# Kernel tuning notes

Measured on AMD Instinct MI355X. Metric: run time of the kernel, lower is better.

The kernel has to match this reference:

```python
import jax, jax.numpy as jnp
import numpy as np

B, L, D, NHEAD, NLAYERS = 2, 2048, 256, 8, 8
NAMES = ['self', 'cross'] * 4


def setup_inputs() -> dict:
    key = jax.random.key(0)
    ks = jax.random.split(key, 6)
    w_scale = D ** -0.5  # keep activations well-scaled
    return {
        'f0': jax.random.normal(ks[0], (B, L, D), dtype=jnp.float32),
        'f1': jax.random.normal(ks[1], (B, L, D), dtype=jnp.float32),
        'Wq': jax.random.normal(ks[2], (NLAYERS, D, D), dtype=jnp.float32) * w_scale,
        'Wk': jax.random.normal(ks[3], (NLAYERS, D, D), dtype=jnp.float32) * w_scale,
        'Wv': jax.random.normal(ks[4], (NLAYERS, D, D), dtype=jnp.float32) * w_scale,
        'Wo': jax.random.normal(ks[5], (NLAYERS, D, D), dtype=jnp.float32) * w_scale,
    }


def _rope(x, inv_freq):
    # x: (B, L, D); RoPE over the FULL model dim (matches original, mixes heads)
    L_, D_ = x.shape[1], x.shape[2]
    t = jnp.arange(L_, dtype=jnp.float32)
    freqs = t[:, None] * inv_freq[None, :]          # (L, D/2)
    emb = jnp.concatenate([freqs, freqs], axis=-1)  # (L, D)
    x1, x2 = x[..., : D_ // 2], x[..., D_ // 2:]
    rot = jnp.concatenate([-x2, x1], axis=-1)
    return x * jnp.cos(emb) + rot * jnp.sin(emb)


def _attn(x, src, wq, wk, wv, wo, use_rope, inv_freq):
    b, l1, d = x.shape
    l2 = src.shape[1]
    dh = d // NHEAD
    q = x @ wq.T    # torch Linear: x @ W^T
    k = src @ wk.T
    v = src @ wv.T
    if use_rope:
        q = _rope(q, inv_freq)
        k = _rope(k, inv_freq)
    q = q.reshape(b, l1, NHEAD, dh)
    k = k.reshape(b, l2, NHEAD, dh)
    v = v.reshape(b, l2, NHEAD, dh)
    scores = jnp.einsum('bqhd,bkhd->bhqk', q, k) * (dh ** -0.5)
    out = jnp.einsum('bhqk,bkhd->bqhd', jax.nn.softmax(scores, axis=-1), v)
    return out.reshape(b, l1, d) @ wo.T


def reference(f0, f1, Wq, Wk, Wv, Wo):
    d = f0.shape[-1]
    inv_freq = 1.0 / (10000.0 ** (jnp.arange(0, d, 2, dtype=jnp.float32) / d))
    for i, name in enumerate(NAMES):
        if name == 'self':
            f0 = f0 + _attn(f0, f0, Wq[i], Wk[i], Wv[i], Wo[i], True, inv_freq)
            f1 = f1 + _attn(f1, f1, Wq[i], Wk[i], Wv[i], Wo[i], True, inv_freq)
        else:
            # sequential updates: second cross uses the UPDATED f0 (matches torch)
            f0 = f0 + _attn(f0, f1, Wq[i], Wk[i], Wv[i], Wo[i], False, inv_freq)
            f1 = f1 + _attn(f1, f0, Wq[i], Wk[i], Wv[i], Wo[i], False, inv_freq)
    return (f0, f1)
```

## Files before the change

kernel.cpp:

```cpp
#include <hip/hip_runtime.h>

#define BB   2
#define LL   2048
#define DD   256
#define NH   8
#define MM   (BB*LL)
#define NLAYERS 8
#define MMDD ((size_t)MM*DD)

typedef unsigned short ushort_t;
typedef __attribute__((ext_vector_type(8))) short  short8;
typedef __attribute__((ext_vector_type(4))) float  f32x4;
typedef __attribute__((ext_vector_type(4))) unsigned int u32x4;
typedef __attribute__((ext_vector_type(2))) unsigned int u32x2;

#define CSC 0.2550500394f

#define WAITV0 asm volatile("s_waitcnt vmcnt(0)" ::: "memory")
#define WAITV2 asm volatile("s_waitcnt vmcnt(2)" ::: "memory")
#define WAITV4 asm volatile("s_waitcnt vmcnt(4)" ::: "memory")
#define WAITV6 asm volatile("s_waitcnt vmcnt(6)" ::: "memory")
#define WAITLG asm volatile("s_waitcnt lgkmcnt(0)" ::: "memory")
#define BAR()  __builtin_amdgcn_s_barrier()
#define SCHED0 __builtin_amdgcn_sched_barrier(0)

__device__ __forceinline__ f32x4 mfma16(short8 a, short8 b, f32x4 c) {
    return __builtin_amdgcn_mfma_f32_16x16x32_bf16(a, b, c, 0, 0, 0);
}
__device__ __forceinline__ unsigned cvtpk(float lo, float hi) {
    unsigned r;
    asm volatile("v_cvt_pk_bf16_f32 %0, %1, %2" : "=v"(r) : "v"(lo), "v"(hi));
    return r;
}
__device__ __forceinline__ void pl32(unsigned &a, unsigned &b) {
    asm volatile("v_permlane32_swap_b32 %0, %1" : "+v"(a), "+v"(b));
}
__device__ __forceinline__ float bf2f(unsigned short h) {
    return __builtin_bit_cast(float, ((unsigned)h) << 16);
}
__device__ __forceinline__ void gll16(const void* gsrc, void* ldst) {
    __builtin_amdgcn_global_load_lds(
        (const __attribute__((address_space(1))) unsigned int*)gsrc,
        (__attribute__((address_space(3))) unsigned int*)ldst, 16, 0, 0);
}


__global__ __launch_bounds__(256) void setup(const float* __restrict__ f0,
                                             const float* __restrict__ f1,
                                             const float* __restrict__ Wq,
                                             const float* __restrict__ Wk,
                                             const float* __restrict__ Wv,
                                             const float* __restrict__ Wo,
                                             float* __restrict__ F,
                                             ushort_t* __restrict__ Fb,
                                             ushort_t* __restrict__ Wb,
                                             float* __restrict__ tab) {
    int b = blockIdx.x, t = threadIdx.x;
    if (b < 1024) {
        int i = b * 256 + t;
        const float* src = (i < 131072) ? f0 : f1;
        int loc = i & 131071;
        const f32x4* p = (const f32x4*)(src + (size_t)loc * 8);
        f32x4 a = p[0], bb = p[1];
        *(f32x4*)&F[(size_t)i * 8]     = a;
        *(f32x4*)&F[(size_t)i * 8 + 4] = bb;
        u32x4 o = {cvtpk(a.x, a.y), cvtpk(a.z, a.w), cvtpk(bb.x, bb.y), cvtpk(bb.z, bb.w)};
        *(u32x4*)&Fb[(size_t)i * 8] = o;
    } else if (b < 2048) {
        int i = (b - 1024) * 256 + t;
        int reg = i >> 16, loc = i & 65535;
        const float* src = reg == 0 ? Wq : reg == 1 ? Wk : reg == 2 ? Wv : Wo;
        const f32x4* p = (const f32x4*)(src + (size_t)loc * 8);
        f32x4 x = p[0], y = p[1];
        u32x4 o = {cvtpk(x.x, x.y), cvtpk(x.z, x.w), cvtpk(y.x, y.y), cvtpk(y.z, y.w)};
        *(u32x4*)&Wb[(size_t)reg * 524288 + (size_t)loc * 8] = o;
    } else {
        int idx = (b - 2048) * 256 + t;
        int p = idx >> 7, j = idx & 127;
        float inv = __expf(-((float)j / 128.f) * 9.210340371976184f);
        float s, c;
        sincosf((float)p * inv, &s, &c);
        tab[(size_t)p * 256 + j]       = c;
        tab[(size_t)p * 256 + 128 + j] = s;
    }
}

__global__ __launch_bounds__(256) void gemmQK(const ushort_t* __restrict__ X,
                                              const ushort_t* __restrict__ WQ,
                                              const ushort_t* __restrict__ WK,
                                              ushort_t* __restrict__ DQ,
                                              ushort_t* __restrict__ KT,
                                              const float* __restrict__ tab) {
    __shared__ ushort_t Xb[2][4096];
    __shared__ ushort_t WbL[2][4096];
    __shared__ ushort_t WbH[2][4096];
    const int tid = threadIdx.x, ln = tid & 63, w = tid >> 6;
    const int f = blockIdx.x;
    const int xcd = f & 7, u = f >> 3;
    const int bx = u & 3, byg = u >> 2;
    const int mat = bx >> 1, cg = bx & 1;
    const int by = xcd * 16 + byg;
    const int m0 = by * 64, n0 = cg * 64;
    const ushort_t* W = mat ? WK : WQ;

    auto stage = [&](int c, int buf) {
#pragma unroll
        for (int i = 0; i < 2; i++) {
            int sl = (w * 2 + i) * 64 + ln;
            int r = sl >> 3, x = sl & 7;
            int col = c * 64 + ((x ^ (r & 7)) << 3);
            gll16(X + (size_t)(m0 + r) * 256 + col,       &Xb[buf][(w * 2 + i) * 512]);
            gll16(W + (size_t)(n0 + r) * 256 + col,       &WbL[buf][(w * 2 + i) * 512]);
            gll16(W + (size_t)(n0 + 128 + r) * 256 + col, &WbH[buf][(w * 2 + i) * 512]);
        }
    };

    const int ql = ln & 15, gq = ln >> 4;
    const int wm = w >> 1, wn = w & 1;
    f32x4 z4 = {0.f, 0.f, 0.f, 0.f};
    f32x4 accL[2][2] = {{z4, z4}, {z4, z4}};
    f32x4 accH[2][2] = {{z4, z4}, {z4, z4}};

    stage(0, 0);
    stage(1, 1);
#pragma unroll
    for (int c = 0; c < 4; c++) {
        if (c < 3) { WAITV6; } else { WAITV0; }
        BAR(); SCHED0;
        const ushort_t* XL = Xb[c & 1];
        const ushort_t* WL = WbL[c & 1];
        const ushort_t* WH = WbH[c & 1];
        __builtin_amdgcn_s_setprio(1);
#pragma unroll
        for (int ks = 0; ks < 2; ks++) {
            int cc = ks * 4 + gq;
            int r0 = 32 * wm + ql, r1 = r0 + 16;
            int nr0 = 32 * wn + ql, nr1 = nr0 + 16;
            short8 a0 = *(const short8*)&XL[(r0 * 8 + (cc ^ (r0 & 7))) * 8];
            short8 a1 = *(const short8*)&XL[(r1 * 8 + (cc ^ (r1 & 7))) * 8];
            short8 l0 = *(const short8*)&WL[(nr0 * 8 + (cc ^ (nr0 & 7))) * 8];
            short8 l1 = *(const short8*)&WL[(nr1 * 8 + (cc ^ (nr1 & 7))) * 8];
            short8 h0 = *(const short8*)&WH[(nr0 * 8 + (cc ^ (nr0 & 7))) * 8];
            short8 h1 = *(const short8*)&WH[(nr1 * 8 + (cc ^ (nr1 & 7))) * 8];
            accL[0][0] = mfma16(a0, l0, accL[0][0]);
            accL[0][1] = mfma16(a0, l1, accL[0][1]);
            accL[1][0] = mfma16(a1, l0, accL[1][0]);
            accL[1][1] = mfma16(a1, l1, accL[1][1]);
            accH[0][0] = mfma16(a0, h0, accH[0][0]);
            accH[0][1] = mfma16(a0, h1, accH[0][1]);
            accH[1][0] = mfma16(a1, h0, accH[1][0]);
            accH[1][1] = mfma16(a1, h1, accH[1][1]);
        }
        __builtin_amdgcn_s_setprio(0);
        BAR();
        if (c + 2 < 4) stage(c + 2, c & 1);
    }

#pragma unroll
    for (int mf = 0; mf < 2; mf++)
#pragma unroll
        for (int nf = 0; nf < 2; nf++)
#pragma unroll
            for (int r = 0; r < 4; r++) {
                int mg = m0 + 32 * wm + 16 * mf + gq * 4 + r;
                int jl = n0 + 32 * wn + 16 * nf + ql;
                int pos = mg & (LL - 1);
                float a = accL[mf][nf][r], b = accH[mf][nf][r];
                float c = tab[(size_t)pos * 256 + jl];
                float s = tab[(size_t)pos * 256 + 128 + jl];
                float o1 = a * c - b * s;
                float o2 = b * c + a * s;
                if (mat == 0) {
                    o1 *= CSC; o2 *= CSC;
                    DQ[(size_t)mg * 256 + jl]       = (ushort_t)cvtpk(o1, o1);
                    DQ[(size_t)mg * 256 + jl + 128] = (ushort_t)cvtpk(o2, o2);
                } else {
                    int z = mg >> 11, key = mg & 2047;
                    int tt = key >> 6, kk = key & 63;
                    int dh = jl & 31, hA = jl >> 5;
                    size_t base = (size_t)tt * 2048 + (size_t)(dh >> 3) * 512
                                + (size_t)kk * 8 + (dh & 7);
                    KT[(size_t)(z * 8 + hA) * 65536 + base]     = (ushort_t)cvtpk(o1, o1);
                    KT[(size_t)(z * 8 + hA + 4) * 65536 + base] = (ushort_t)cvtpk(o2, o2);
                }
            }
}

template<int NQ, int NK, int NV, int QMODE, int KMODE, int NTY>
__global__ __launch_bounds__(256) void gemm5(const ushort_t* __restrict__ X,
                                             const ushort_t* __restrict__ WQ,
                                             const ushort_t* __restrict__ WK,
                                             const ushort_t* __restrict__ WV,
                                             ushort_t* __restrict__ DQ,
                                             ushort_t* __restrict__ DK,
                                             ushort_t* __restrict__ DVT) {
    constexpr int NTX = NQ + NK + NV;
    __shared__ ushort_t Xb[3][4096];
    __shared__ ushort_t Wb[3][4096];
    const int tid = threadIdx.x, ln = tid & 63, w = tid >> 6;
    const int f = blockIdx.x;
    const int xcd = f & 7, s = f >> 3;
    const int bx = s % NTX, byg = s / NTX;
    const int by = xcd * (NTY / 8) + byg;
    const int m0 = by * 64;

    const ushort_t* W; ushort_t* DH; int n0, mode;
    if (NQ && bx < NQ)           { W = WQ; DH = DQ;  mode = QMODE; n0 = bx * 64; }
    else if (NK && bx < NQ + NK) { W = WK; DH = DK;  mode = KMODE; n0 = (bx - NQ) * 64; }
    else                         { W = WV; DH = DVT; mode = 3; n0 = (bx - NQ - NK) * 64; }

    auto stage = [&](int c, int buf) {
#pragma unroll
        for (int i = 0; i < 2; i++) {
            int sl = (w * 2 + i) * 64 + ln;
            int r = sl >> 3, x = sl & 7;
            int col = c * 64 + ((x ^ (r & 7)) << 3);
            gll16(X + (size_t)(m0 + r) * 256 + col, &Xb[buf][(w * 2 + i) * 512]);
            gll16(W + (size_t)(n0 + r) * 256 + col, &Wb[buf][(w * 2 + i) * 512]);
        }
    };

    const int ql = ln & 15, gq = ln >> 4;
    const int wm = w >> 1, wn = w & 1;
    f32x4 z4 = {0.f, 0.f, 0.f, 0.f};
    f32x4 acc[2][2] = {{z4, z4}, {z4, z4}};

    stage(0, 0);
    stage(1, 1);
#pragma unroll
    for (int c = 0; c < 4; c++) {
        if (c < 3) { WAITV4; } else { WAITV0; }
        BAR(); SCHED0;
        if (c + 2 < 4) stage(c + 2, (c + 2) % 3);
        const ushort_t* XL = Xb[c % 3];
        const ushort_t* WL = Wb[c % 3];
        __builtin_amdgcn_s_setprio(1);
#pragma unroll
        for (int ks = 0; ks < 2; ks++) {
            int cc = ks * 4 + gq;
            int r0 = 32 * wm + ql, r1 = r0 + 16;
            int nr0 = 32 * wn + ql, nr1 = nr0 + 16;
            short8 a0 = *(const short8*)&XL[(r0 * 8 + (cc ^ (r0 & 7))) * 8];
            short8 a1 = *(const short8*)&XL[(r1 * 8 + (cc ^ (r1 & 7))) * 8];
            short8 b0 = *(const short8*)&WL[(nr0 * 8 + (cc ^ (nr0 & 7))) * 8];
            short8 b1 = *(const short8*)&WL[(nr1 * 8 + (cc ^ (nr1 & 7))) * 8];
            acc[0][0] = mfma16(a0, b0, acc[0][0]);
            acc[0][1] = mfma16(a0, b1, acc[0][1]);
            acc[1][0] = mfma16(a1, b0, acc[1][0]);
            acc[1][1] = mfma16(a1, b1, acc[1][1]);
        }
        __builtin_amdgcn_s_setprio(0);
    }

    if (mode == 3) {
        float* scr = (float*)&Xb[0][0];
        __syncthreads();
#pragma unroll
        for (int mf = 0; mf < 2; mf++)
#pragma unroll
            for (int nf = 0; nf < 2; nf++)
#pragma unroll
                for (int r = 0; r < 4; r++) {
                    int nloc = 32 * wn + 16 * nf + ql;
                    int mloc = 32 * wm + 16 * mf + 4 * gq + r;
                    scr[nloc * 65 + mloc] = acc[mf][nf][r];
                }
        __syncthreads();
        int nloc = tid >> 2, mc = (tid & 3) * 16;
        int ng = n0 + nloc, hh = ng >> 5, dh = ng & 31;
        int mg = m0 + mc;
        int z = mg >> 11, key = mg & 2047;
        int tt = key >> 6;
        int ks = (mc >> 5) & 1, J = (mc >> 4) & 1;
        int cA = 4 * ks + 2 * J, cB = cA + 1;
        int swz = dh & 7;
        const float* sc = &scr[nloc * 65 + mc];
        u32x2 q0 = {cvtpk(sc[0], sc[1]),   cvtpk(sc[2], sc[3])};
        u32x2 q1 = {cvtpk(sc[4], sc[5]),   cvtpk(sc[6], sc[7])};
        u32x2 q2 = {cvtpk(sc[8], sc[9]),   cvtpk(sc[10], sc[11])};
        u32x2 q3 = {cvtpk(sc[12], sc[13]), cvtpk(sc[14], sc[15])};
        ushort_t* base = &DVT[(size_t)(z * 8 + hh) * 65536 + (size_t)tt * 2048 + dh * 64];
        *(u32x2*)&base[(cA ^ swz) * 8]     = q0;
        *(u32x2*)&base[(cB ^ swz) * 8]     = q1;
        *(u32x2*)&base[(cA ^ swz) * 8 + 4] = q2;
        *(u32x2*)&base[(cB ^ swz) * 8 + 4] = q3;
    } else {
#pragma unroll
        for (int mf = 0; mf < 2; mf++)
#pragma unroll
            for (int nf = 0; nf < 2; nf++)
#pragma unroll
                for (int r = 0; r < 4; r++) {
                    int mg = m0 + 32 * wm + 16 * mf + gq * 4 + r;
                    int ng = n0 + 32 * wn + 16 * nf + ql;
                    float v = acc[mf][nf][r];
                    if (mode == 2) {
                        DH[(size_t)mg * 256 + ng] = (ushort_t)cvtpk(v, v);
                    } else if (mode == 5) {
                        int zh = (mg >> 11) * 8 + (ng >> 5);
                        size_t off = (size_t)zh * 65536
                                   + (size_t)((mg & 2047) >> 6) * 2048
                                   + (size_t)((ng & 31) >> 3) * 512
                                   + (size_t)(mg & 63) * 8 + (ng & 7);
                        DH[off] = (ushort_t)cvtpk(v, v);
                    } else {
                        float vs = v * CSC;
                        DH[(size_t)mg * 256 + ng] = (ushort_t)cvtpk(vs, vs);
                    }
                }
    }
}

template<int SPLIT, int NTY>
__global__ __launch_bounds__(256) void gemmO(const float* __restrict__ Op,
                                             const float* __restrict__ Lp,
                                             const ushort_t* __restrict__ W,
                                             const float* __restrict__ Res,
                                             float* __restrict__ OutF,
                                             ushort_t* __restrict__ OutH,
                                             int mrows) {
    __shared__ ushort_t Xf[64 * 256];
    __shared__ ushort_t Wpb[3][4096];
    const int tid = threadIdx.x, ln = tid & 63, w = tid >> 6;
    const int f = blockIdx.x;
    const int xcd = f & 7, s = f >> 3;
    const int bx = s & 3, byg = s >> 2;
    const int by = xcd * (NTY / 8) + byg;
    const int m0 = by * 64, n0 = bx * 64;

    auto stageW = [&](int c, int buf) {
#pragma unroll
        for (int i = 0; i < 2; i++) {
            int sl = (w * 2 + i) * 64 + ln;
            int r = sl >> 3, x = sl & 7;
            int col = c * 64 + ((x ^ (r & 7)) << 3);
            gll16(W + (size_t)(n0 + r) * 256 + col, &Wpb[buf][(w * 2 + i) * 512]);
        }
    };
    stageW(0, 0);
    stageW(1, 1);

    const int xr = tid >> 2, q = tid & 3, hb = q >> 1;
    float inv[4];
#pragma unroll
    for (int hh = 0; hh < 4; hh++) {
        float l = 0.f;
#pragma unroll
        for (int sp = 0; sp < SPLIT; sp++)
            l += Lp[(size_t)sp * mrows * 8 + (size_t)(m0 + xr) * 8 + 2 * hh + hb];
        inv[hh] = 1.f / l;
    }
#pragma unroll
    for (int p = 0; p < 4; p++) {
        int col = q * 16 + 64 * p;
        f32x4 a0 = {0.f,0.f,0.f,0.f}, a1 = a0, a2 = a0, a3 = a0;
#pragma unroll
        for (int sp = 0; sp < SPLIT; sp++) {
            const float* src = &Op[(size_t)sp * mrows * 256 + (size_t)(m0 + xr) * 256 + col];
            a0 += *(const f32x4*)&src[0];
            a1 += *(const f32x4*)&src[4];
            a2 += *(const f32x4*)&src[8];
            a3 += *(const f32x4*)&src[12];
        }
        float iv = inv[p];
        a0 *= iv; a1 *= iv; a2 *= iv; a3 *= iv;
        u32x4 w0 = {cvtpk(a0.x, a0.y), cvtpk(a0.z, a0.w),
                    cvtpk(a1.x, a1.y), cvtpk(a1.z, a1.w)};
        u32x4 w1 = {cvtpk(a2.x, a2.y), cvtpk(a2.z, a2.w),
                    cvtpk(a3.x, a3.y), cvtpk(a3.z, a3.w)};
        int xc0 = q * 2;
        *(u32x4*)&Xf[xr * 256 + p * 64 + ((xc0)     ^ (xr & 7)) * 8] = w0;
        *(u32x4*)&Xf[xr * 256 + p * 64 + ((xc0 + 1) ^ (xr & 7)) * 8] = w1;
    }
    WAITLG;
    BAR(); SCHED0;

    const int ql = ln & 15, gq = ln >> 4;
    const int wm = w >> 1, wn = w & 1;
    f32x4 z4 = {0.f, 0.f, 0.f, 0.f};
    f32x4 acc[2][2] = {{z4, z4}, {z4, z4}};
#pragma unroll
    for (int c = 0; c < 4; c++) {
        if (c < 3) { WAITV2; } else { WAITV0; }
        BAR(); SCHED0;
        if (c + 2 < 4) stageW(c + 2, (c + 2) % 3);
        const ushort_t* WL = Wpb[c % 3];
        __builtin_amdgcn_s_setprio(1);
#pragma unroll
        for (int ks = 0; ks < 2; ks++) {
            int cc = ks * 4 + gq;
            int r0 = 32 * wm + ql, r1 = r0 + 16;
            int nr0 = 32 * wn + ql, nr1 = nr0 + 16;
            short8 a0 = *(const short8*)&Xf[r0 * 256 + c * 64 + (cc ^ (r0 & 7)) * 8];
            short8 a1 = *(const short8*)&Xf[r1 * 256 + c * 64 + (cc ^ (r1 & 7)) * 8];
            short8 b0 = *(const short8*)&WL[(nr0 * 8 + (cc ^ (nr0 & 7))) * 8];
            short8 b1 = *(const short8*)&WL[(nr1 * 8 + (cc ^ (nr1 & 7))) * 8];
            acc[0][0] = mfma16(a0, b0, acc[0][0]);
            acc[0][1] = mfma16(a0, b1, acc[0][1]);
            acc[1][0] = mfma16(a1, b0, acc[1][0]);
            acc[1][1] = mfma16(a1, b1, acc[1][1]);
        }
        __builtin_amdgcn_s_setprio(0);
    }

#pragma unroll
    for (int mf = 0; mf < 2; mf++)
#pragma unroll
        for (int nf = 0; nf < 2; nf++)
#pragma unroll
            for (int r = 0; r < 4; r++) {
                int mg = m0 + 32 * wm + 16 * mf + gq * 4 + r;
                int ng = n0 + 32 * wn + 16 * nf + ql;
                size_t idx = (size_t)mg * 256 + ng;
                float o = Res[idx] + acc[mf][nf][r];
                OutF[idx] = o;
                OutH[idx] = (ushort_t)cvtpk(o, o);
            }
}

template<int SPLIT>
__global__ __launch_bounds__(256) void attn9(const ushort_t* __restrict__ Q,
                                             const ushort_t* __restrict__ K,
                                             const ushort_t* __restrict__ Vt,
                                             float* __restrict__ Op,
                                             float* __restrict__ Lp, int mrows) {
    constexpr int KEYS = 2048 / SPLIT;
    constexpr int NP = KEYS / 128;
    __shared__ ushort_t K_lds[2][4096];
    __shared__ ushort_t V_lds[2][4096];

    const int tid = threadIdx.x, ln = tid & 63, w = tid >> 6;
    const int ql = ln & 15, gq = ln >> 4;
    const int f = blockIdx.x;
    const int xcd = f & 7, slot = f >> 3;
    const int qb = slot & 15, gg = slot >> 4;
    const int h = xcd;
    const int zz = gg / SPLIT, sp = gg % SPLIT;
    const int q0 = qb * 128 + w * 32;
    const size_t rb = (size_t)zz * 2048;
    const int zh = zz * 8 + h;

    short8 qfA = *(const short8*)&Q[(rb + q0 + ql) * 256 + h * 32 + gq * 8];
    short8 qfB = *(const short8*)&Q[(rb + q0 + 16 + ql) * 256 + h * 32 + gq * 8];

    const ushort_t* kt = K  + (size_t)zh * 65536 + (size_t)sp * (KEYS / 64) * 2048
                            + w * 1024 + ln * 8;
    const ushort_t* vt = Vt + (size_t)zh * 65536 + (size_t)sp * (KEYS / 64) * 2048
                            + w * 1024 + ln * 8;

    auto stage = [&](int p, int buf) {
        gll16(kt + (size_t)p * 4096,       &K_lds[buf][w * 1024]);
        gll16(kt + (size_t)p * 4096 + 512, &K_lds[buf][w * 1024 + 512]);
        gll16(vt + (size_t)p * 4096,       &V_lds[buf][w * 1024]);
        gll16(vt + (size_t)p * 4096 + 512, &V_lds[buf][w * 1024 + 512]);
    };
    stage(0, 0);
    stage(1, 1);

    const short os = (short)0x3F80;
    const short8 ones = {os, os, os, os, os, os, os, os};
    f32x4 z4 = {0.f, 0.f, 0.f, 0.f};
    f32x4 o0A = z4, o1A = z4, o0B = z4, o1B = z4, laccA = z4, laccB = z4;

    for (int p = 0; p < NP; p++) {
        if (p < NP - 1) { WAITV4; } else { WAITV0; }
        BAR(); SCHED0;
        const ushort_t* KL = K_lds[p & 1];
        const ushort_t* VL = V_lds[p & 1];

        short8 pA[4], pB[4];
#pragma unroll
        for (int h2 = 0; h2 < 2; h2++) {
            const ushort_t* KLh = KL + h2 * 2048;
            f32x4 sA[4], sB[4];
            __builtin_amdgcn_s_setprio(1);
#pragma unroll
            for (int jj = 0; jj < 4; jj++) {
                short8 kf = *(const short8*)&KLh[(gq * 64 + 16 * jj + ql) * 8];
                sA[jj] = mfma16(kf, qfA, z4);
                sB[jj] = mfma16(kf, qfB, z4);
            }
            __builtin_amdgcn_s_setprio(0);
#pragma unroll
            for (int jj = 0; jj < 4; jj++)
#pragma unroll
                for (int r = 0; r < 4; r++) {
                    sA[jj][r] = __builtin_amdgcn_exp2f(sA[jj][r]);
                    sB[jj][r] = __builtin_amdgcn_exp2f(sB[jj][r]);
                }
            unsigned aLo[4], aHi[4], bLo[4], bHi[4];
#pragma unroll
            for (int jj = 0; jj < 4; jj++) {
                aLo[jj] = cvtpk(sA[jj][0], sA[jj][1]);
                aHi[jj] = cvtpk(sA[jj][2], sA[jj][3]);
                bLo[jj] = cvtpk(sB[jj][0], sB[jj][1]);
                bHi[jj] = cvtpk(sB[jj][2], sB[jj][3]);
            }
            pl32(aLo[0], aLo[1]); pl32(aHi[0], aHi[1]);
            pl32(aLo[2], aLo[3]); pl32(aHi[2], aHi[3]);
            pl32(bLo[0], bLo[1]); pl32(bHi[0], bHi[1]);
            pl32(bLo[2], bLo[3]); pl32(bHi[2], bHi[3]);
            u32x4 fA0 = {aLo[0], aHi[0], aLo[1], aHi[1]};
            u32x4 fA1 = {aLo[2], aHi[2], aLo[3], aHi[3]};
            u32x4 fB0 = {bLo[0], bHi[0], bLo[1], bHi[1]};
            u32x4 fB1 = {bLo[2], bHi[2], bLo[3], bHi[3]};
            pA[h2 * 2]     = __builtin_bit_cast(short8, fA0);
            pA[h2 * 2 + 1] = __builtin_bit_cast(short8, fA1);
            pB[h2 * 2]     = __builtin_bit_cast(short8, fB0);
            pB[h2 * 2 + 1] = __builtin_bit_cast(short8, fB1);
        }

        __builtin_amdgcn_s_setprio(1);
#pragma unroll
        for (int ks = 0; ks < 4; ks++) {
            int img = ks >> 1, ks2 = ks & 1;
            int sw = (4 * ks2 + gq) ^ (ql & 7);
            short8 vf0 = *(const short8*)&VL[img * 2048 + (ql * 8 + sw) * 8];
            short8 vf1 = *(const short8*)&VL[img * 2048 + ((16 + ql) * 8 + sw) * 8];
            o0A = mfma16(vf0, pA[ks], o0A);
            o1A = mfma16(vf1, pA[ks], o1A);
            o0B = mfma16(vf0, pB[ks], o0B);
            o1B = mfma16(vf1, pB[ks], o1B);
            laccA = mfma16(ones, pA[ks], laccA);
            laccB = mfma16(ones, pB[ks], laccB);
        }
        __builtin_amdgcn_s_setprio(0);

        if (p + 2 < NP) {
            BAR();
            stage(p + 2, p & 1);
        }
    }

    size_t rowA = rb + q0 + ql, rowB = rowA + 16;
    float* obA = Op + (size_t)sp * mrows * 256 + rowA * 256 + h * 32;
    float* obB = Op + (size_t)sp * mrows * 256 + rowB * 256 + h * 32;
    *(f32x4*)&obA[gq * 4]      = o0A;
    *(f32x4*)&obA[16 + gq * 4] = o1A;
    *(f32x4*)&obB[gq * 4]      = o0B;
    *(f32x4*)&obB[16 + gq * 4] = o1B;
    if (gq == 0) {
        Lp[(size_t)sp * mrows * 8 + rowA * 8 + h] = laccA[0];
        Lp[(size_t)sp * mrows * 8 + rowB * 8 + h] = laccB[0];
    }
}

extern "C" void kernel_launch(void* const* d_in, const int* in_sizes, int n_in,
                              void* d_out, int out_size, void* d_ws, size_t ws_size,
                              hipStream_t stream) {
    const float* f0_in = (const float*)d_in[0];
    const float* f1_in = (const float*)d_in[1];
    const float* Wq = (const float*)d_in[2];
    const float* Wk = (const float*)d_in[3];
    const float* Wv = (const float*)d_in[4];
    const float* Wo = (const float*)d_in[5];

    float* F0 = (float*)d_out;
    float* F1 = F0 + MMDD;

    ushort_t* Fb  = (ushort_t*)d_ws;
    ushort_t* Qb  = Fb  + 2 * MMDD;
    ushort_t* Khb = Qb  + 2 * MMDD;
    ushort_t* Vhb = Khb + 2 * MMDD;
    ushort_t* Wb  = Vhb + 2 * MMDD;
    float*    Opw = (float*)(Wb + 2 * MMDD);
    float*    Lpw = Opw + (size_t)4 * MMDD;
    float*    tab = Lpw + 262144;

    ushort_t* Wqb = Wb;
    ushort_t* Wkb = Wb + (size_t)NLAYERS * 65536;
    ushort_t* Wvb = Wb + (size_t)2 * NLAYERS * 65536;
    ushort_t* Wob = Wb + (size_t)3 * NLAYERS * 65536;

    setup<<<3072, 256, 0, stream>>>(f0_in, f1_in, Wq, Wk, Wv, Wo, F0, Fb, Wb, tab);

    for (int i = 0; i < NLAYERS; i++) {
        const ushort_t* wq = Wqb + (size_t)i * 65536;
        const ushort_t* wk = Wkb + (size_t)i * 65536;
        const ushort_t* wv = Wvb + (size_t)i * 65536;
        const ushort_t* wo = Wob + (size_t)i * 65536;

        if ((i & 1) == 0) {
            gemmQK<<<512, 256, 0, stream>>>(Fb, wq, wk, Qb, Khb, tab);
            gemm5<0, 0, 4, 0, 0, 128><<<512, 256, 0, stream>>>(
                Fb, nullptr, nullptr, wv, nullptr, nullptr, Vhb);
            attn9<2><<<1024, 256, 0, stream>>>(Qb, Khb, Vhb, Opw, Lpw, MM * 2);
            gemmO<2, 128><<<512, 256, 0, stream>>>(Opw, Lpw, wo, F0, F0, Fb, MM * 2);
        } else {
            gemm5<4, 0, 0, 4, 0, 128><<<512, 256, 0, stream>>>(
                Fb, wq, nullptr, nullptr, Qb, nullptr, nullptr);
            for (int s = 0; s < 2; s++) {
                const ushort_t* sb = Fb + (size_t)(1 - s) * MMDD;
                float* xf = s ? F1 : F0;
                ushort_t* xbw = Fb + (size_t)s * MMDD;
                gemm5<0, 4, 4, 0, 5, 64><<<512, 256, 0, stream>>>(
                    sb, nullptr, wk, wv, nullptr, Khb, Vhb);
                attn9<4><<<1024, 256, 0, stream>>>(Qb + (size_t)s * MMDD,
                                                   Khb, Vhb, Opw, Lpw, MM);
                gemmO<4, 64><<<256, 256, 0, stream>>>(Opw, Lpw, wo, xf, xf, xbw, MM);
            }
        }
    }
}
```

Measured before the change: 560.0 us.

## Split attention over more key chunks with bf16 partials and triple-buffered 64-key tiles

The attention kernel now processes 64-key tiles with a three-stage LDS ring and a single barrier per tile, and splits the keys into 3 chunks for self layers and 8 for cross layers, launching more blocks. Partial outputs are written as bf16 instead of fp32, halving partial-buffer traffic, and the output projection kernel converts them back while reducing the larger number of splits. This aims to raise occupancy and parallelism and cut memory traffic, at the cost of more reduction work and reduced precision in the partial sums.

```diff
diff --git a/kernel.cpp b/kernel.cpp
--- a/kernel.cpp
+++ b/kernel.cpp
@@ -312,7 +312,7 @@
 }
 
 template<int SPLIT, int NTY>
-__global__ __launch_bounds__(256) void gemmO(const float* __restrict__ Op,
+__global__ __launch_bounds__(256) void gemmO(const ushort_t* __restrict__ Opb,
                                              const float* __restrict__ Lp,
                                              const ushort_t* __restrict__ W,
                                              const float* __restrict__ Res,
@@ -356,11 +356,18 @@
         f32x4 a0 = {0.f,0.f,0.f,0.f}, a1 = a0, a2 = a0, a3 = a0;
 #pragma unroll
         for (int sp = 0; sp < SPLIT; sp++) {
-            const float* src = &Op[(size_t)sp * mrows * 256 + (size_t)(m0 + xr) * 256 + col];
-            a0 += *(const f32x4*)&src[0];
-            a1 += *(const f32x4*)&src[4];
-            a2 += *(const f32x4*)&src[8];
-            a3 += *(const f32x4*)&src[12];
+            const ushort_t* src = &Opb[((size_t)sp * mrows + m0 + xr) * 256 + col];
+            u32x4 v0 = *(const u32x4*)&src[0];
+            u32x4 v1 = *(const u32x4*)&src[8];
+            f32x4 b0 = {bf2f(v0.x & 0xffff), bf2f(v0.x >> 16),
+                        bf2f(v0.y & 0xffff), bf2f(v0.y >> 16)};
+            f32x4 b1 = {bf2f(v0.z & 0xffff), bf2f(v0.z >> 16),
+                        bf2f(v0.w & 0xffff), bf2f(v0.w >> 16)};
+            f32x4 b2 = {bf2f(v1.x & 0xffff), bf2f(v1.x >> 16),
+                        bf2f(v1.y & 0xffff), bf2f(v1.y >> 16)};
+            f32x4 b3 = {bf2f(v1.z & 0xffff), bf2f(v1.z >> 16),
+                        bf2f(v1.w & 0xffff), bf2f(v1.w >> 16)};
+            a0 += b0; a1 += b1; a2 += b2; a3 += b3;
         }
         float iv = inv[p];
         a0 *= iv; a1 *= iv; a2 *= iv; a3 *= iv;
@@ -419,15 +426,13 @@
 }
 
 template<int SPLIT>
-__global__ __launch_bounds__(256) void attn9(const ushort_t* __restrict__ Q,
-                                             const ushort_t* __restrict__ K,
-                                             const ushort_t* __restrict__ Vt,
-                                             float* __restrict__ Op,
-                                             float* __restrict__ Lp, int mrows) {
-    constexpr int KEYS = 2048 / SPLIT;
-    constexpr int NP = KEYS / 128;
-    __shared__ ushort_t K_lds[2][4096];
-    __shared__ ushort_t V_lds[2][4096];
+__global__ __launch_bounds__(256, 6) void attn10(const ushort_t* __restrict__ Q,
+                                                 const ushort_t* __restrict__ K,
+                                                 const ushort_t* __restrict__ Vt,
+                                                 ushort_t* __restrict__ Opb,
+                                                 float* __restrict__ Lp, int mrows) {
+    __shared__ ushort_t K_lds[3][2048];
+    __shared__ ushort_t V_lds[3][2048];
 
     const int tid = threadIdx.x, ln = tid & 63, w = tid >> 6;
     const int ql = ln & 15, gq = ln >> 4;
@@ -436,6 +441,8 @@
     const int qb = slot & 15, gg = slot >> 4;
     const int h = xcd;
     const int zz = gg / SPLIT, sp = gg % SPLIT;
+    const int t0 = (sp * 32) / SPLIT;
+    const int NT = ((sp + 1) * 32) / SPLIT - t0;
     const int q0 = qb * 128 + w * 32;
     const size_t rb = (size_t)zz * 2048;
     const int zh = zz * 8 + h;
@@ -443,102 +450,98 @@
     short8 qfA = *(const short8*)&Q[(rb + q0 + ql) * 256 + h * 32 + gq * 8];
     short8 qfB = *(const short8*)&Q[(rb + q0 + 16 + ql) * 256 + h * 32 + gq * 8];
 
-    const ushort_t* kt = K  + (size_t)zh * 65536 + (size_t)sp * (KEYS / 64) * 2048
-                            + w * 1024 + ln * 8;
-    const ushort_t* vt = Vt + (size_t)zh * 65536 + (size_t)sp * (KEYS / 64) * 2048
-                            + w * 1024 + ln * 8;
-
-    auto stage = [&](int p, int buf) {
-        gll16(kt + (size_t)p * 4096,       &K_lds[buf][w * 1024]);
-        gll16(kt + (size_t)p * 4096 + 512, &K_lds[buf][w * 1024 + 512]);
-        gll16(vt + (size_t)p * 4096,       &V_lds[buf][w * 1024]);
-        gll16(vt + (size_t)p * 4096 + 512, &V_lds[buf][w * 1024 + 512]);
-    };
-    stage(0, 0);
-    stage(1, 1);
+    const ushort_t* kt = K  + (size_t)zh * 65536 + (size_t)t0 * 2048 + tid * 8;
+    const ushort_t* vt = Vt + (size_t)zh * 65536 + (size_t)t0 * 2048 + tid * 8;
+
+    gll16(kt,        &K_lds[0][w * 512]);
+    gll16(vt,        &V_lds[0][w * 512]);
+    gll16(kt + 2048, &K_lds[1][w * 512]);
+    gll16(vt + 2048, &V_lds[1][w * 512]);
 
     const short os = (short)0x3F80;
     const short8 ones = {os, os, os, os, os, os, os, os};
     f32x4 z4 = {0.f, 0.f, 0.f, 0.f};
     f32x4 o0A = z4, o1A = z4, o0B = z4, o1B = z4, laccA = z4, laccB = z4;
 
-    for (int p = 0; p < NP; p++) {
-        if (p < NP - 1) { WAITV4; } else { WAITV0; }
+    int cur = 0, pre = 2;
+    for (int t = 0; t < NT; t++) {
+        if (t < NT - 1) { WAITV2; } else { WAITV0; }
         BAR(); SCHED0;
-        const ushort_t* KL = K_lds[p & 1];
-        const ushort_t* VL = V_lds[p & 1];
-
-        short8 pA[4], pB[4];
-#pragma unroll
-        for (int h2 = 0; h2 < 2; h2++) {
-            const ushort_t* KLh = KL + h2 * 2048;
-            f32x4 sA[4], sB[4];
-            __builtin_amdgcn_s_setprio(1);
-#pragma unroll
-            for (int jj = 0; jj < 4; jj++) {
-                short8 kf = *(const short8*)&KLh[(gq * 64 + 16 * jj + ql) * 8];
-                sA[jj] = mfma16(kf, qfA, z4);
-                sB[jj] = mfma16(kf, qfB, z4);
+        if (t + 2 < NT) {
+            gll16(kt + (size_t)(t + 2) * 2048, &K_lds[pre][w * 512]);
+            gll16(vt + (size_t)(t + 2) * 2048, &V_lds[pre][w * 512]);
+        }
+        const ushort_t* KL = K_lds[cur];
+        const ushort_t* VL = V_lds[cur];
+
+        f32x4 stA[4], stB[4];
+        __builtin_amdgcn_s_setprio(1);
+#pragma unroll
+        for (int j = 0; j < 4; j++) {
+            short8 kf = *(const short8*)&KL[(gq * 64 + 16 * j + ql) * 8];
+            stA[j] = mfma16(kf, qfA, z4);
+            stB[j] = mfma16(kf, qfB, z4);
+        }
+        __builtin_amdgcn_s_setprio(0);
+#pragma unroll
+        for (int j = 0; j < 4; j++)
+#pragma unroll
+            for (int r = 0; r < 4; r++) {
+                stA[j][r] = __builtin_amdgcn_exp2f(stA[j][r]);
+                stB[j][r] = __builtin_amdgcn_exp2f(stB[j][r]);
             }
-            __builtin_amdgcn_s_setprio(0);
-#pragma unroll
-            for (int jj = 0; jj < 4; jj++)
-#pragma unroll
-                for (int r = 0; r < 4; r++) {
-                    sA[jj][r] = __builtin_amdgcn_exp2f(sA[jj][r]);
-                    sB[jj][r] = __builtin_amdgcn_exp2f(sB[jj][r]);
-                }
-            unsigned aLo[4], aHi[4], bLo[4], bHi[4];
-#pragma unroll
-            for (int jj = 0; jj < 4; jj++) {
-                aLo[jj] = cvtpk(sA[jj][0], sA[jj][1]);
-                aHi[jj] = cvtpk(sA[jj][2], sA[jj][3]);
-                bLo[jj] = cvtpk(sB[jj][0], sB[jj][1]);
-                bHi[jj] = cvtpk(sB[jj][2], sB[jj][3]);
-            }
-            pl32(aLo[0], aLo[1]); pl32(aHi[0], aHi[1]);
-            pl32(aLo[2], aLo[3]); pl32(aHi[2], aHi[3]);
-            pl32(bLo[0], bLo[1]); pl32(bHi[0], bHi[1]);
-            pl32(bLo[2], bLo[3]); pl32(bHi[2], bHi[3]);
-            u32x4 fA0 = {aLo[0], aHi[0], aLo[1], aHi[1]};
-            u32x4 fA1 = {aLo[2], aHi[2], aLo[3], aHi[3]};
-            u32x4 fB0 = {bLo[0], bHi[0], bLo[1], bHi[1]};
-            u32x4 fB1 = {bLo[2], bHi[2], bLo[3], bHi[3]};
-            pA[h2 * 2]     = __builtin_bit_cast(short8, fA0);
-            pA[h2 * 2 + 1] = __builtin_bit_cast(short8, fA1);
-            pB[h2 * 2]     = __builtin_bit_cast(short8, fB0);
-            pB[h2 * 2 + 1] = __builtin_bit_cast(short8, fB1);
-        }
+        unsigned aLo[4], aHi[4], bLo[4], bHi[4];
+#pragma unroll
+        for (int j = 0; j < 4; j++) {
+            aLo[j] = cvtpk(stA[j][0], stA[j][1]);
+            aHi[j] = cvtpk(stA[j][2], stA[j][3]);
+            bLo[j] = cvtpk(stB[j][0], stB[j][1]);
+            bHi[j] = cvtpk(stB[j][2], stB[j][3]);
+        }
+        pl32(aLo[0], aLo[1]); pl32(aHi[0], aHi[1]);
+        pl32(aLo[2], aLo[3]); pl32(aHi[2], aHi[3]);
+        pl32(bLo[0], bLo[1]); pl32(bHi[0], bHi[1]);
+        pl32(bLo[2], bLo[3]); pl32(bHi[2], bHi[3]);
+        u32x4 fA0 = {aLo[0], aHi[0], aLo[1], aHi[1]};
+        u32x4 fA1 = {aLo[2], aHi[2], aLo[3], aHi[3]};
+        u32x4 fB0 = {bLo[0], bHi[0], bLo[1], bHi[1]};
+        u32x4 fB1 = {bLo[2], bHi[2], bLo[3], bHi[3]};
+        short8 pfA0 = __builtin_bit_cast(short8, fA0);
+        short8 pfA1 = __builtin_bit_cast(short8, fA1);
+        short8 pfB0 = __builtin_bit_cast(short8, fB0);
+        short8 pfB1 = __builtin_bit_cast(short8, fB1);
 
         __builtin_amdgcn_s_setprio(1);
 #pragma unroll
-        for (int ks = 0; ks < 4; ks++) {
-            int img = ks >> 1, ks2 = ks & 1;
-            int sw = (4 * ks2 + gq) ^ (ql & 7);
-            short8 vf0 = *(const short8*)&VL[img * 2048 + (ql * 8 + sw) * 8];
-            short8 vf1 = *(const short8*)&VL[img * 2048 + ((16 + ql) * 8 + sw) * 8];
-            o0A = mfma16(vf0, pA[ks], o0A);
-            o1A = mfma16(vf1, pA[ks], o1A);
-            o0B = mfma16(vf0, pB[ks], o0B);
-            o1B = mfma16(vf1, pB[ks], o1B);
-            laccA = mfma16(ones, pA[ks], laccA);
-            laccB = mfma16(ones, pB[ks], laccB);
+        for (int ks = 0; ks < 2; ks++) {
+            int sw = (4 * ks + gq) ^ (ql & 7);
+            short8 vf0 = *(const short8*)&VL[(ql * 8 + sw) * 8];
+            short8 vf1 = *(const short8*)&VL[((16 + ql) * 8 + sw) * 8];
+            short8 pA = ks ? pfA1 : pfA0;
+            short8 pB = ks ? pfB1 : pfB0;
+            o0A = mfma16(vf0, pA, o0A);
+            o1A = mfma16(vf1, pA, o1A);
+            o0B = mfma16(vf0, pB, o0B);
+            o1B = mfma16(vf1, pB, o1B);
+            laccA = mfma16(ones, pA, laccA);
+            laccB = mfma16(ones, pB, laccB);
         }
         __builtin_amdgcn_s_setprio(0);
-
-        if (p + 2 < NP) {
-            BAR();
-            stage(p + 2, p & 1);
-        }
+        cur = (cur == 2) ? 0 : cur + 1;
+        pre = (pre == 2) ? 0 : pre + 1;
     }
 
     size_t rowA = rb + q0 + ql, rowB = rowA + 16;
-    float* obA = Op + (size_t)sp * mrows * 256 + rowA * 256 + h * 32;
-    float* obB = Op + (size_t)sp * mrows * 256 + rowB * 256 + h * 32;
-    *(f32x4*)&obA[gq * 4]      = o0A;
-    *(f32x4*)&obA[16 + gq * 4] = o1A;
-    *(f32x4*)&obB[gq * 4]      = o0B;
-    *(f32x4*)&obB[16 + gq * 4] = o1B;
+    ushort_t* obA = Opb + ((size_t)sp * mrows + rowA) * 256 + h * 32;
+    ushort_t* obB = Opb + ((size_t)sp * mrows + rowB) * 256 + h * 32;
+    u32x2 wA0 = {cvtpk(o0A.x, o0A.y), cvtpk(o0A.z, o0A.w)};
+    u32x2 wA1 = {cvtpk(o1A.x, o1A.y), cvtpk(o1A.z, o1A.w)};
+    u32x2 wB0 = {cvtpk(o0B.x, o0B.y), cvtpk(o0B.z, o0B.w)};
+    u32x2 wB1 = {cvtpk(o1B.x, o1B.y), cvtpk(o1B.z, o1B.w)};
+    *(u32x2*)&obA[gq * 4]      = wA0;
+    *(u32x2*)&obA[16 + gq * 4] = wA1;
+    *(u32x2*)&obB[gq * 4]      = wB0;
+    *(u32x2*)&obB[16 + gq * 4] = wB1;
     if (gq == 0) {
         Lp[(size_t)sp * mrows * 8 + rowA * 8 + h] = laccA[0];
         Lp[(size_t)sp * mrows * 8 + rowB * 8 + h] = laccB[0];
@@ -563,8 +566,8 @@
     ushort_t* Khb = Qb  + 2 * MMDD;
     ushort_t* Vhb = Khb + 2 * MMDD;
     ushort_t* Wb  = Vhb + 2 * MMDD;
-    float*    Opw = (float*)(Wb + 2 * MMDD);
-    float*    Lpw = Opw + (size_t)4 * MMDD;
+    ushort_t* Opb = Wb  + 2 * MMDD;
+    float*    Lpw = (float*)(Opb + 8 * MMDD);
     float*    tab = Lpw + 262144;
 
     ushort_t* Wqb = Wb;
@@ -584,8 +587,8 @@
             gemmQK<<<512, 256, 0, stream>>>(Fb, wq, wk, Qb, Khb, tab);
             gemm5<0, 0, 4, 0, 0, 128><<<512, 256, 0, stream>>>(
                 Fb, nullptr, nullptr, wv, nullptr, nullptr, Vhb);
-            attn9<2><<<1024, 256, 0, stream>>>(Qb, Khb, Vhb, Opw, Lpw, MM * 2);
-            gemmO<2, 128><<<512, 256, 0, stream>>>(Opw, Lpw, wo, F0, F0, Fb, MM * 2);
+            attn10<3><<<1536, 256, 0, stream>>>(Qb, Khb, Vhb, Opb, Lpw, MM * 2);
+            gemmO<3, 128><<<512, 256, 0, stream>>>(Opb, Lpw, wo, F0, F0, Fb, MM * 2);
         } else {
             gemm5<4, 0, 0, 4, 0, 128><<<512, 256, 0, stream>>>(
                 Fb, wq, nullptr, nullptr, Qb, nullptr, nullptr);
@@ -595,9 +598,9 @@
                 ushort_t* xbw = Fb + (size_t)s * MMDD;
                 gemm5<0, 4, 4, 0, 5, 64><<<512, 256, 0, stream>>>(
                     sb, nullptr, wk, wv, nullptr, Khb, Vhb);
-                attn9<4><<<1024, 256, 0, stream>>>(Qb + (size_t)s * MMDD,
-                                                   Khb, Vhb, Opw, Lpw, MM);
-                gemmO<4, 64><<<256, 256, 0, stream>>>(Opw, Lpw, wo, xf, xf, xbw, MM);
+                attn10<8><<<2048, 256, 0, stream>>>(Qb + (size_t)s * MMDD,
+                                                    Khb, Vhb, Opb, Lpw, MM);
+                gemmO<8, 64><<<256, 256, 0, stream>>>(Opb, Lpw, wo, xf, xf, xbw, MM);
             }
         }
     }
```

After: 513.5 us. 8.3% less time.
